# Performance work log

Measured on AMD Instinct MI355X. Metric: run time of the kernel, lower is better.

Reference implementation:

```python
import jax, jax.numpy as jnp
import numpy as np

B, N, D, H, C = 8, 1024, 1024, 8, 1
S = 32            # sqrt(D // C): per-patch spatial map side
HD = D // H       # head dim = 128
SCALE = HD ** -0.5
BN_EPS = 1e-3     # Keras BatchNormalization default epsilon


def setup_inputs() -> dict:
    key = jax.random.key(0)
    ks = jax.random.split(key, 7)
    std = 0.02  # matches tf.random_normal_initializer(0.0, 0.02)
    return {
        "x": jax.random.normal(ks[0], (B, N, D), jnp.float32),
        "qw": jax.random.normal(ks[1], (3, 3, C, C), jnp.float32) * std,
        "kw": jax.random.normal(ks[2], (3, 3, C, C), jnp.float32) * std,
        "vw": jax.random.normal(ks[3], (3, 3, C, C), jnp.float32) * std,
        "reatten_w": jax.random.normal(ks[4], (N, N), jnp.float32) / np.float32(np.sqrt(N)),
        "reatten_b": jnp.zeros((N,), jnp.float32),
        "bn_gamma": jnp.ones((N,), jnp.float32),
        "bn_beta": jnp.zeros((N,), jnp.float32),
        "proj_w": jax.random.normal(ks[5], (D, D), jnp.float32) / np.float32(np.sqrt(D)),
        "proj_b": jnp.zeros((D,), jnp.float32),
    }


def _conv_qkv(x, w):
    # unflatten: [B, N, D] -> [B*N, S, S, C]; map_fn over batch with a shared
    # conv == one conv with B*N as batch dim. 3x3 SAME, no bias, exact GELU.
    xm = x.reshape(B * N, S, S, C)
    y = jax.lax.conv_general_dilated(
        xm, w, window_strides=(1, 1), padding='SAME',
        dimension_numbers=('NHWC', 'HWIO', 'NHWC'))
    y = jax.nn.gelu(y, approximate=False)
    # reshape to heads: [B, N, H, HD] -> [B, H, N, HD]
    return y.reshape(B, N, H, HD).transpose(0, 2, 1, 3)


def reference(x, qw, kw, vw, reatten_w, reatten_b, bn_gamma, bn_beta, proj_w, proj_b):
    q = _conv_qkv(x, qw)
    k = _conv_qkv(x, kw)
    v = _conv_qkv(x, vw)

    attn = jax.nn.softmax(jnp.einsum('bhid,bhjd->bhij', q, k) * SCALE, axis=-1)
    # re-attention: 1x1 conv over last (key) axis + BN (inference: mean=0, var=1)
    attn = jnp.einsum('bhic,cj->bhij', attn, reatten_w) + reatten_b
    attn = attn * (bn_gamma / jnp.sqrt(jnp.float32(1.0) + BN_EPS)) + bn_beta
    # reatten_scale = 1.0 (transform_scale=False)

    out = jnp.einsum('bhij,bhjd->bhid', attn, v)
    out = out.transpose(0, 2, 1, 3).reshape(B, N, D)
    out = out @ proj_w + proj_b
    return (out, attn)
```

## Files before the change

kernel.cpp:

```cpp
#include <hip/hip_runtime.h>
#include <hip/hip_bf16.h>

typedef __attribute__((ext_vector_type(8))) short short8;
typedef __attribute__((ext_vector_type(4))) float f32x4;

__device__ __forceinline__ void gload_lds16(const void* g, void* l) {
    __builtin_amdgcn_global_load_lds(
        (const __attribute__((address_space(1))) void*)g,
        (__attribute__((address_space(3))) void*)l, 16, 0, 0);
}

__device__ __forceinline__ float gelu_exact(float x) {
    return 0.5f * x * (1.0f + erff(x * 0.70710678118654752f));
}
__device__ __forceinline__ unsigned short f2b_raw(float f) {
    __hip_bfloat16 h = __float2bfloat16(f);
    return *reinterpret_cast<unsigned short*>(&h);
}
__device__ __forceinline__ float tofloat(float f) { return f; }
__device__ __forceinline__ float tofloat(__hip_bfloat16 h) { return __bfloat162float(h); }

__global__ __launch_bounds__(256) void conv_qkv(
    const float* __restrict__ x,
    const float* __restrict__ qw, const float* __restrict__ kw, const float* __restrict__ vw,
    __hip_bfloat16* __restrict__ qb, __hip_bfloat16* __restrict__ kb, __hip_bfloat16* __restrict__ vb)
{
    __shared__ float img[1024];
    const int bid = blockIdx.x;
    const int b = bid >> 10, n = bid & 1023;
    const float* xr = x + (long)bid * 1024;
    for (int i = threadIdx.x; i < 1024; i += 256) img[i] = xr[i];
    __syncthreads();

    float wq[9], wk[9], wv[9];
    #pragma unroll
    for (int i = 0; i < 9; ++i) { wq[i] = qw[i]; wk[i] = kw[i]; wv[i] = vw[i]; }

    for (int q = 0; q < 4; ++q) {
        const int p = q * 256 + threadIdx.x;
        const int r = p >> 5, c = p & 31;
        float sq = 0.f, sk = 0.f, sv = 0.f;
        #pragma unroll
        for (int dy = 0; dy < 3; ++dy) {
            const int rr = r + dy - 1;
            if (rr < 0 || rr > 31) continue;
            #pragma unroll
            for (int dx = 0; dx < 3; ++dx) {
                const int cc = c + dx - 1;
                if (cc < 0 || cc > 31) continue;
                const float px = img[rr * 32 + cc];
                sq += px * wq[dy * 3 + dx];
                sk += px * wk[dy * 3 + dx];
                sv += px * wv[dy * 3 + dx];
            }
        }
        sq = gelu_exact(sq); sk = gelu_exact(sk); sv = gelu_exact(sv);
        const int h = p >> 7, d = p & 127;
        const long off = ((long)(b * 8 + h) * 1024 + n) * 128 + d;
        qb[off] = __float2bfloat16(sq);
        kb[off] = __float2bfloat16(sk);
        vb[off] = __float2bfloat16(sv);
    }
}

template <typename Tin>
__global__ __launch_bounds__(256) void transpose_cast(
    const Tin* __restrict__ in, __hip_bfloat16* __restrict__ out,
    int R, int Cc, long inz, long outz)
{
    __shared__ float tile[32][33];
    const long z = blockIdx.z;
    const int c0 = blockIdx.x * 32, r0 = blockIdx.y * 32;
    const int tx = threadIdx.x & 31, ty = threadIdx.x >> 5;
    const Tin* ip = in + z * inz;
    #pragma unroll
    for (int i = 0; i < 32; i += 8)
        tile[ty + i][tx] = tofloat(ip[(long)(r0 + ty + i) * Cc + (c0 + tx)]);
    __syncthreads();
    __hip_bfloat16* op = out + z * outz;
    #pragma unroll
    for (int i = 0; i < 32; i += 8)
        op[(long)(c0 + ty + i) * R + (r0 + tx)] = __float2bfloat16(tile[tx][ty + i]);
}

__global__ __launch_bounds__(256, 2) void qk_softmax(
    const __hip_bfloat16* __restrict__ qb, const __hip_bfloat16* __restrict__ kb,
    __hip_bfloat16* __restrict__ Pun, float* __restrict__ linv)
{
    __shared__ __align__(16) char smem[74240];
    char* As = smem;
    char* Bs = smem + 32768;
    __hip_bfloat16* pbuf = (__hip_bfloat16*)(smem + 65536);
    float* lred = (float*)(smem + 65536);

    const int tid = threadIdx.x;
    const int rt = blockIdx.x, z = blockIdx.y;
    const char* Ag = (const char*)(qb + ((long)z * 1024 + rt * 128) * 128);
    const char* Bg = (const char*)(kb + (long)z * 1024 * 128);

    int gsrc[8], pphys[8];
    #pragma unroll
    for (int i = 0; i < 8; ++i) {
        const int p = i * 4096 + tid * 16;
        const int L = p ^ (((p >> 8) & 7) << 4);
        pphys[i] = p; gsrc[i] = L;
    }
    auto STAGE = [&](const char* gb, char* lb) {
        #pragma unroll
        for (int i = 0; i < 8; ++i) gload_lds16(gb + gsrc[i], lb + pphys[i]);
    };
    auto LD8 = [&](const char* buf, int L) -> short8 {
        const int ph = L ^ (((L >> 8) & 7) << 4);
        return *(const short8*)(buf + ph);
    };

    const int lane = tid & 63, wave = tid >> 6;
    const int wr = (wave >> 1) * 64, wc = (wave & 1) * 64;
    const int fr = lane & 15, kl = lane >> 4;

    STAGE(Ag, As);
    STAGE(Bg, Bs);
    __syncthreads();

    short8 af[4][4];
    #pragma unroll
    for (int m = 0; m < 4; ++m)
        #pragma unroll
        for (int kk = 0; kk < 4; ++kk)
            af[m][kk] = LD8(As, (wr + m * 16 + fr) * 256 + (kl * 8 + kk * 32) * 2);

    float lacc[4][4];
    #pragma unroll
    for (int m = 0; m < 4; ++m)
        #pragma unroll
        for (int r = 0; r < 4; ++r) lacc[m][r] = 0.f;

    const float SCALE = 0.08838834764831843f;

    for (int c = 0; c < 8; ++c) {
        f32x4 acc[4][4];
        #pragma unroll
        for (int m = 0; m < 4; ++m)
            #pragma unroll
            for (int n = 0; n < 4; ++n) acc[m][n] = (f32x4){0.f, 0.f, 0.f, 0.f};

        #pragma unroll
        for (int kk = 0; kk < 4; ++kk) {
            short8 bf[4];
            #pragma unroll
            for (int n = 0; n < 4; ++n)
                bf[n] = LD8(Bs, (wc + n * 16 + fr) * 256 + (kl * 8 + kk * 32) * 2);
            #pragma unroll
            for (int m = 0; m < 4; ++m)
                #pragma unroll
                for (int n = 0; n < 4; ++n)
                    acc[m][n] = __builtin_amdgcn_mfma_f32_16x16x32_bf16(af[m][kk], bf[n], acc[m][n], 0, 0, 0);
        }

        #pragma unroll
        for (int m = 0; m < 4; ++m) {
            #pragma unroll
            for (int n = 0; n < 4; ++n)
                #pragma unroll
                for (int r = 0; r < 4; ++r)
                    acc[m][n][r] = __expf(acc[m][n][r] * SCALE);
            #pragma unroll
            for (int r = 0; r < 4; ++r)
                lacc[m][r] += (acc[m][0][r] + acc[m][1][r]) + (acc[m][2][r] + acc[m][3][r]);
        }

        #pragma unroll
        for (int q2 = 0; q2 < 4; ++q2) {
            if ((wave >> 1) == (q2 >> 1)) {
                #pragma unroll
                for (int mm = 0; mm < 2; ++mm) {
                    const int m = (q2 & 1) * 2 + mm;
                    const int lr0 = m * 16 + kl * 4 - (q2 & 1) * 32;
                    #pragma unroll
                    for (int n = 0; n < 4; ++n)
                        #pragma unroll
                        for (int r = 0; r < 4; ++r)
                            pbuf[(lr0 + r) * 136 + wc + n * 16 + fr] = __float2bfloat16(acc[m][n][r]);
                }
            }
            __syncthreads();
            #pragma unroll
            for (int p = 0; p < 2; ++p) {
                const int idx = (tid + p * 256) * 8;
                const int row = idx >> 7, col = idx & 127;
                short8 s = *(const short8*)&pbuf[row * 136 + col];
                *(short8*)&Pun[((long)z * 1024 + rt * 128 + q2 * 32 + row) * 1024 + c * 128 + col] = s;
            }
            __syncthreads();
        }

        if (c < 7) {
            STAGE(Bg + (c + 1) * 32768, Bs);
            __syncthreads();
        }
    }

    #pragma unroll
    for (int m = 0; m < 4; ++m)
        #pragma unroll
        for (int r = 0; r < 4; ++r) {
            float v = lacc[m][r];
            v += __shfl_xor(v, 1); v += __shfl_xor(v, 2);
            v += __shfl_xor(v, 4); v += __shfl_xor(v, 8);
            lacc[m][r] = v;
        }
    __syncthreads();
    if (fr == 0) {
        #pragma unroll
        for (int m = 0; m < 4; ++m)
            #pragma unroll
            for (int r = 0; r < 4; ++r)
                lred[(wr + m * 16 + kl * 4 + r) * 2 + (wave & 1)] = lacc[m][r];
    }
    __syncthreads();
    if (tid < 128) {
        const float s = lred[tid * 2] + lred[tid * 2 + 1];
        linv[(long)z * 1024 + rt * 128 + tid] = 1.0f / s;
    }
}

__global__ __launch_bounds__(512, 2) void gemm_reatten_256(
    const __hip_bfloat16* __restrict__ Sall, const __hip_bfloat16* __restrict__ Wt,
    float* __restrict__ Cout, __hip_bfloat16* __restrict__ C2out,
    const float* __restrict__ bg, const float* __restrict__ rb, const float* __restrict__ bb,
    const float* __restrict__ linv)
{
    __shared__ __align__(16) char smem[131072];
    char* ldsA = smem;
    char* ldsB = smem + 65536;

    const int tid = threadIdx.x;
    const int h = blockIdx.x + (blockIdx.y << 2) + (blockIdx.z << 4);
    const int lg = (h & 7) * 128 + (h >> 3);
    const int z = lg >> 4, tileM = lg & 3, tileN = (lg >> 2) & 3;

    const char* Ab = (const char*)(Sall + (long)z * 1048576 + (long)tileM * 256 * 1024);
    const char* Bb = (const char*)(Wt + (long)tileN * 256 * 1024);

    int grow[2], goff[2], pphys[2];
    #pragma unroll
    for (int i = 0; i < 2; ++i) {
        const int p = i * 8192 + tid * 16;
        const int l = p ^ (((p >> 7) & 3) << 4);
        pphys[i] = p; grow[i] = l >> 6; goff[i] = l & 63;
    }
    auto STAGE = [&](const char* gb, char* lb, int kt) {
        #pragma unroll
        for (int i = 0; i < 2; ++i)
            gload_lds16(gb + (long)grow[i] * 2048 + kt * 64 + goff[i], lb + pphys[i]);
    };

    const int lane = tid & 63, wid = tid >> 6;
    const int wrM = wid >> 2, wcn = wid & 3;
    const int fr = lane & 15, kl = lane >> 4;
    const int frbase = fr * 64 + kl * 16;

    auto LD8 = [&](const char* buf, int L) -> short8 {
        const int ph = L ^ (((L >> 7) & 3) << 4);
        return *(const short8*)(buf + ph);
    };

    f32x4 acc[8][4];
    #pragma unroll
    for (int m = 0; m < 8; ++m)
        #pragma unroll
        for (int n = 0; n < 4; ++n) acc[m][n] = (f32x4){0.f, 0.f, 0.f, 0.f};

    STAGE(Ab, ldsA, 0);          STAGE(Bb, ldsB, 0);
    STAGE(Ab, ldsA + 16384, 1);  STAGE(Bb, ldsB + 16384, 1);
    asm volatile("s_waitcnt vmcnt(4)" ::: "memory");
    __builtin_amdgcn_sched_barrier(0);
    __builtin_amdgcn_s_barrier();
    __builtin_amdgcn_sched_barrier(0);

    #pragma unroll 1
    for (int t = 0; t < 32; ++t) {
        char* bufA = ldsA + (t & 3) * 16384;
        char* bufB = ldsB + (t & 3) * 16384;
        const int t2 = t + 2;
        char* nA = ldsA + (t2 & 3) * 16384;
        char* nB = ldsB + (t2 & 3) * 16384;

        short8 bf[4], af[4], ag[4];
        #pragma unroll
        for (int n = 0; n < 4; ++n) bf[n] = LD8(bufB, ((wcn * 64 + n * 16) * 64) + frbase);
        #pragma unroll
        for (int j = 0; j < 4; ++j) af[j] = LD8(bufA, ((wrM * 128 + j * 16) * 64) + frbase);
        if (t2 < 32) STAGE(Ab, nA, t2);
        __builtin_amdgcn_s_setprio(1);
        #pragma unroll
        for (int j = 0; j < 4; ++j)
            #pragma unroll
            for (int n = 0; n < 4; ++n)
                acc[j][n] = __builtin_amdgcn_mfma_f32_16x16x32_bf16(af[j], bf[n], acc[j][n], 0, 0, 0);
        __builtin_amdgcn_s_setprio(0);

        #pragma unroll
        for (int j = 0; j < 4; ++j) ag[j] = LD8(bufA, ((wrM * 128 + 64 + j * 16) * 64) + frbase);
        if (t2 < 32) STAGE(Bb, nB, t2);
        __builtin_amdgcn_s_setprio(1);
        #pragma unroll
        for (int j = 0; j < 4; ++j)
            #pragma unroll
            for (int n = 0; n < 4; ++n)
                acc[4 + j][n] = __builtin_amdgcn_mfma_f32_16x16x32_bf16(ag[j], bf[n], acc[4 + j][n], 0, 0, 0);
        __builtin_amdgcn_s_setprio(0);

        if (t < 30)       { asm volatile("s_waitcnt vmcnt(4)" ::: "memory"); }
        else if (t == 30) { asm volatile("s_waitcnt vmcnt(0)" ::: "memory"); }
        __builtin_amdgcn_sched_barrier(0);
        __builtin_amdgcn_s_barrier();
        __builtin_amdgcn_sched_barrier(0);
    }

    __syncthreads();
    float* cbuf = (float*)smem;
    const float bninv = rsqrtf(1.0f + 1e-3f);
    float alpha[4], addv[4];
    #pragma unroll
    for (int n = 0; n < 4; ++n) {
        const int col = tileN * 256 + wcn * 64 + n * 16 + fr;
        const float g = bg[col];
        alpha[n] = g * bninv;
        addv[n] = rb[col] * alpha[n] + bb[col];
    }
    const float* linvz = linv + (long)z * 1024 + tileM * 256 + wrM * 128 + kl * 4;
    f32x4 lr[8];
    #pragma unroll
    for (int mf = 0; mf < 8; ++mf) lr[mf] = *(const f32x4*)(linvz + mf * 16);

    const int srow = tid >> 3, cseg = (tid & 7) * 4, c8 = (tid & 7) * 8;
    #pragma unroll
    for (int c = 0; c < 4; ++c) {
        if (wrM == (c >> 1)) {
            #pragma unroll
            for (int j = 0; j < 4; ++j) {
                const int mf = (c & 1) * 4 + j;
                const int lrow0 = j * 16 + kl * 4;
                #pragma unroll
                for (int n = 0; n < 4; ++n)
                    #pragma unroll
                    for (int r = 0; r < 4; ++r)
                        cbuf[(lrow0 + r) * 260 + wcn * 64 + n * 16 + fr] =
                            acc[mf][n][r] * (lr[mf][r] * alpha[n]) + addv[n];
            }
        }
        __syncthreads();
        const long gro = (long)(tileM * 256 + c * 64 + srow);
        float* gp = Cout + (long)z * 1048576 + gro * 1024 + tileN * 256;
        #pragma unroll
        for (int i = 0; i < 8; ++i)
            *(f32x4*)(gp + cseg + i * 32) = *(const f32x4*)&cbuf[srow * 260 + cseg + i * 32];
        __hip_bfloat16* gp2 = C2out + (long)z * 1048576 + gro * 1024 + tileN * 256;
        #pragma unroll
        for (int i = 0; i < 4; ++i) {
            const float* src = &cbuf[srow * 260 + c8 + i * 64];
            f32x4 v0 = *(const f32x4*)src;
            f32x4 v1 = *(const f32x4*)(src + 4);
            short8 s;
            #pragma unroll
            for (int k = 0; k < 4; ++k) {
                s[k] = (short)f2b_raw(v0[k]);
                s[k + 4] = (short)f2b_raw(v1[k]);
            }
            *(short8*)(gp2 + c8 + i * 64) = s;
        }
        __syncthreads();
    }
}

template <int MODE>
__global__ __launch_bounds__(256) void gemm_nt(
    const __hip_bfloat16* __restrict__ Aall, const __hip_bfloat16* __restrict__ Ball,
    void* __restrict__ Call, int K,
    long sAz, long sBz, long sCz,
    const float* __restrict__ e0)
{
    constexpr bool OF32 = (MODE == 3);

    __shared__ __align__(16) char smem[32 * 132 * 4];
    short* As = (short*)smem;
    short* Bs = (short*)(smem + 8192);
    float* cbuf = (float*)smem;

    const int tid = threadIdx.x;
    const int z = blockIdx.z;
    const int tileM = blockIdx.x, tileN = blockIdx.y;

    const short* Aw = (const short*)Aall + sAz * z + (long)tileM * 128 * K;
    const short* Bw = (const short*)Ball + sBz * z + (long)tileN * 128 * K;

    const int r0s = tid >> 2, k0s = (tid & 3) * 8;
    const int r1s = r0s + 64;

    f32x4 acc[4][4];
    #pragma unroll
    for (int m = 0; m < 4; ++m)
        #pragma unroll
        for (int n = 0; n < 4; ++n) acc[m][n] = (f32x4){0.f, 0.f, 0.f, 0.f};

    const int lane = tid & 63;
    const int wave = tid >> 6;
    const int wr = (wave >> 1) * 64, wc = (wave & 1) * 64;
    const int fr = lane & 15;
    const int kb = (lane >> 4) * 8;

    const int nk = K >> 5;
    for (int kt = 0; kt < nk; ++kt) {
        __syncthreads();
        gload_lds16(Aw + (long)r0s * K + kt * 32 + k0s, &As[tid * 8]);
        gload_lds16(Aw + (long)r1s * K + kt * 32 + k0s, &As[(tid + 256) * 8]);
        gload_lds16(Bw + (long)r0s * K + kt * 32 + k0s, &Bs[tid * 8]);
        gload_lds16(Bw + (long)r1s * K + kt * 32 + k0s, &Bs[(tid + 256) * 8]);
        __syncthreads();

        short8 af[4], bf[4];
        #pragma unroll
        for (int m = 0; m < 4; ++m) af[m] = *(const short8*)&As[(wr + m * 16 + fr) * 32 + kb];
        #pragma unroll
        for (int n = 0; n < 4; ++n) bf[n] = *(const short8*)&Bs[(wc + n * 16 + fr) * 32 + kb];
        #pragma unroll
        for (int m = 0; m < 4; ++m)
            #pragma unroll
            for (int n = 0; n < 4; ++n)
                acc[m][n] = __builtin_amdgcn_mfma_f32_16x16x32_bf16(af[m], bf[n], acc[m][n], 0, 0, 0);
    }

    long cbase;
    if (MODE == 2) cbase = (long)(z >> 3) * 1048576 + (long)(z & 7) * 128;
    else           cbase = sCz * z;

    float addv[4];
    #pragma unroll
    for (int n = 0; n < 4; ++n) {
        const int col = tileN * 128 + wc + n * 16 + fr;
        addv[n] = (MODE == 3) ? e0[col] : 0.f;
    }

    __syncthreads();
    #pragma unroll
    for (int q = 0; q < 4; ++q) {
        if ((wave >> 1) == (q >> 1)) {
            #pragma unroll
            for (int mm = 0; mm < 2; ++mm) {
                const int m = (q & 1) * 2 + mm;
                const int lr0 = m * 16 + (lane >> 4) * 4 - (q & 1) * 32;
                #pragma unroll
                for (int n = 0; n < 4; ++n)
                    #pragma unroll
                    for (int r = 0; r < 4; ++r)
                        cbuf[(lr0 + r) * 132 + wc + n * 16 + fr] = acc[m][n][r] + addv[n];
            }
        }
        __syncthreads();
        const long growbase = (long)tileM * 128 + q * 32;
        if constexpr (OF32) {
            float* Cg = (float*)Call + cbase;
            #pragma unroll
            for (int pass = 0; pass < 4; ++pass) {
                const int idx = (tid + pass * 256) * 4;
                const int row = idx >> 7, col = idx & 127;
                f32x4 v = *(const f32x4*)&cbuf[row * 132 + col];
                *(f32x4*)&Cg[(growbase + row) * 1024 + tileN * 128 + col] = v;
            }
        } else {
            __hip_bfloat16* Cg = (__hip_bfloat16*)Call + cbase;
            #pragma unroll
            for (int pass = 0; pass < 2; ++pass) {
                const int idx = (tid + pass * 256) * 8;
                const int row = idx >> 7, col = idx & 127;
                const float* src = &cbuf[row * 132 + col];
                f32x4 v0 = *(const f32x4*)src;
                f32x4 v1 = *(const f32x4*)(src + 4);
                short8 s;
                #pragma unroll
                for (int i = 0; i < 4; ++i) {
                    s[i] = (short)f2b_raw(v0[i]);
                    s[i + 4] = (short)f2b_raw(v1[i]);
                }
                *(short8*)&Cg[(growbase + row) * 1024 + tileN * 128 + col] = s;
            }
        }
        __syncthreads();
    }
}

extern "C" void kernel_launch(void* const* d_in, const int* in_sizes, int n_in,
                              void* d_out, int out_size, void* d_ws, size_t ws_size,
                              hipStream_t stream)
{
    const float* x  = (const float*)d_in[0];
    const float* qw = (const float*)d_in[1];
    const float* kw = (const float*)d_in[2];
    const float* vw = (const float*)d_in[3];
    const float* rw = (const float*)d_in[4];
    const float* rb = (const float*)d_in[5];
    const float* bg = (const float*)d_in[6];
    const float* bb = (const float*)d_in[7];
    const float* pw = (const float*)d_in[8];
    const float* pb = (const float*)d_in[9];

    float* outF  = (float*)d_out;
    float* attnF = outF + 8388608;

    char* w = (char*)d_ws;
    __hip_bfloat16* qb    = (__hip_bfloat16*)w; w += 16777216;
    __hip_bfloat16* kb    = (__hip_bfloat16*)w; w += 16777216;
    __hip_bfloat16* vb    = (__hip_bfloat16*)w; w += 16777216;
    __hip_bfloat16* vt    = (__hip_bfloat16*)w; w += 16777216;
    __hip_bfloat16* Wt    = (__hip_bfloat16*)w; w += 2097152;
    __hip_bfloat16* pWt   = (__hip_bfloat16*)w; w += 2097152;
    __hip_bfloat16* o2    = (__hip_bfloat16*)w; w += 16777216;
    float*          linv  = (float*)w;          w += 262144;
    __hip_bfloat16* Pun   = (__hip_bfloat16*)w; w += 134217728;
    __hip_bfloat16* attnb = (__hip_bfloat16*)w; w += 134217728;

    conv_qkv<<<8192, 256, 0, stream>>>(x, qw, kw, vw, qb, kb, vb);
    transpose_cast<float><<<dim3(32, 32, 1), 256, 0, stream>>>(rw, Wt, 1024, 1024, 0, 0);
    transpose_cast<float><<<dim3(32, 32, 1), 256, 0, stream>>>(pw, pWt, 1024, 1024, 0, 0);
    transpose_cast<__hip_bfloat16><<<dim3(4, 32, 64), 256, 0, stream>>>(vb, vt, 1024, 128, 131072, 131072);

    qk_softmax<<<dim3(8, 64), 256, 0, stream>>>(qb, kb, Pun, linv);
    gemm_reatten_256<<<dim3(4, 4, 64), 512, 0, stream>>>(Pun, Wt, attnF, attnb, bg, rb, bb, linv);
    gemm_nt<2><<<dim3(8, 1, 64), 256, 0, stream>>>(
        attnb, vt, o2, 1024, 1048576, 131072, 0, nullptr);
    gemm_nt<3><<<dim3(64, 8, 1), 256, 0, stream>>>(
        o2, pWt, outF, 1024, 0, 0, 0, pb);
}
```

Before: 397.4 us.

## Restructure reatten GEMM to double-buffered K=64 stages with plain block mapping

The reatten GEMM kernel moves from a 4-deep ring of K=32 LDS stages, with two loads in flight and explicit vmcnt waits, to a double-buffered scheme of K=64 stages. It runs 16 iterations with a wider XOR swizzle and __syncthreads between iterations. The swizzled grid-to-tile remapping is replaced by a direct blockIdx mapping, and launch bounds drop the two-blocks-per-CU hint. This cuts barrier count and loop overhead, but it gives up one stage of prefetch depth and the L2-locality remap, and the full-barrier waits may expose more load latency.

```diff
diff --git a/kernel.cpp b/kernel.cpp
--- a/kernel.cpp
+++ b/kernel.cpp
@@ -224,7 +224,7 @@
     }
 }
 
-__global__ __launch_bounds__(512, 2) void gemm_reatten_256(
+__global__ __launch_bounds__(512, 1) void gemm_reatten_256(
     const __hip_bfloat16* __restrict__ Sall, const __hip_bfloat16* __restrict__ Wt,
     float* __restrict__ Cout, __hip_bfloat16* __restrict__ C2out,
     const float* __restrict__ bg, const float* __restrict__ rb, const float* __restrict__ bb,
@@ -235,33 +235,29 @@
     char* ldsB = smem + 65536;
 
     const int tid = threadIdx.x;
-    const int h = blockIdx.x + (blockIdx.y << 2) + (blockIdx.z << 4);
-    const int lg = (h & 7) * 128 + (h >> 3);
-    const int z = lg >> 4, tileM = lg & 3, tileN = (lg >> 2) & 3;
-
+    const int z = blockIdx.z, tileM = blockIdx.x, tileN = blockIdx.y;
     const char* Ab = (const char*)(Sall + (long)z * 1048576 + (long)tileM * 256 * 1024);
     const char* Bb = (const char*)(Wt + (long)tileN * 256 * 1024);
 
-    int grow[2], goff[2], pphys[2];
-    #pragma unroll
-    for (int i = 0; i < 2; ++i) {
+    int gsrow[4], gscol[4], pphys[4];
+    #pragma unroll
+    for (int i = 0; i < 4; ++i) {
         const int p = i * 8192 + tid * 16;
-        const int l = p ^ (((p >> 7) & 3) << 4);
-        pphys[i] = p; grow[i] = l >> 6; goff[i] = l & 63;
+        const int L = p ^ (((p >> 7) & 7) << 4);
+        pphys[i] = p; gsrow[i] = L >> 7; gscol[i] = L & 127;
     }
     auto STAGE = [&](const char* gb, char* lb, int kt) {
         #pragma unroll
-        for (int i = 0; i < 2; ++i)
-            gload_lds16(gb + (long)grow[i] * 2048 + kt * 64 + goff[i], lb + pphys[i]);
+        for (int i = 0; i < 4; ++i)
+            gload_lds16(gb + (long)gsrow[i] * 2048 + kt * 128 + gscol[i], lb + pphys[i]);
     };
 
     const int lane = tid & 63, wid = tid >> 6;
     const int wrM = wid >> 2, wcn = wid & 3;
     const int fr = lane & 15, kl = lane >> 4;
-    const int frbase = fr * 64 + kl * 16;
 
     auto LD8 = [&](const char* buf, int L) -> short8 {
-        const int ph = L ^ (((L >> 7) & 3) << 4);
+        const int ph = L ^ (((L >> 7) & 7) << 4);
         return *(const short8*)(buf + ph);
     };
 
@@ -271,54 +267,58 @@
         #pragma unroll
         for (int n = 0; n < 4; ++n) acc[m][n] = (f32x4){0.f, 0.f, 0.f, 0.f};
 
-    STAGE(Ab, ldsA, 0);          STAGE(Bb, ldsB, 0);
-    STAGE(Ab, ldsA + 16384, 1);  STAGE(Bb, ldsB + 16384, 1);
-    asm volatile("s_waitcnt vmcnt(4)" ::: "memory");
-    __builtin_amdgcn_sched_barrier(0);
-    __builtin_amdgcn_s_barrier();
-    __builtin_amdgcn_sched_barrier(0);
+    STAGE(Ab, ldsA, 0);
+    STAGE(Bb, ldsB, 0);
+    __syncthreads();
 
     #pragma unroll 1
-    for (int t = 0; t < 32; ++t) {
-        char* bufA = ldsA + (t & 3) * 16384;
-        char* bufB = ldsB + (t & 3) * 16384;
-        const int t2 = t + 2;
-        char* nA = ldsA + (t2 & 3) * 16384;
-        char* nB = ldsB + (t2 & 3) * 16384;
-
-        short8 bf[4], af[4], ag[4];
-        #pragma unroll
-        for (int n = 0; n < 4; ++n) bf[n] = LD8(bufB, ((wcn * 64 + n * 16) * 64) + frbase);
-        #pragma unroll
-        for (int j = 0; j < 4; ++j) af[j] = LD8(bufA, ((wrM * 128 + j * 16) * 64) + frbase);
-        if (t2 < 32) STAGE(Ab, nA, t2);
+    for (int t = 0; t < 16; ++t) {
+        char* bufA = ldsA + (t & 1) * 32768;
+        char* bufB = ldsB + (t & 1) * 32768;
+        char* nA = ldsA + ((t + 1) & 1) * 32768;
+        char* nB = ldsB + ((t + 1) & 1) * 32768;
+
+        short8 bf[4][2], af[4][2];
+        #pragma unroll
+        for (int n = 0; n < 4; ++n)
+            #pragma unroll
+            for (int ks = 0; ks < 2; ++ks)
+                bf[n][ks] = LD8(bufB, (wcn * 64 + n * 16 + fr) * 128 + ks * 64 + kl * 16);
+        #pragma unroll
+        for (int j = 0; j < 4; ++j)
+            #pragma unroll
+            for (int ks = 0; ks < 2; ++ks)
+                af[j][ks] = LD8(bufA, (wrM * 128 + j * 16 + fr) * 128 + ks * 64 + kl * 16);
+        if (t < 15) STAGE(Ab, nA, t + 1);
         __builtin_amdgcn_s_setprio(1);
         #pragma unroll
         for (int j = 0; j < 4; ++j)
             #pragma unroll
-            for (int n = 0; n < 4; ++n)
-                acc[j][n] = __builtin_amdgcn_mfma_f32_16x16x32_bf16(af[j], bf[n], acc[j][n], 0, 0, 0);
+            for (int n = 0; n < 4; ++n) {
+                acc[j][n] = __builtin_amdgcn_mfma_f32_16x16x32_bf16(af[j][0], bf[n][0], acc[j][n], 0, 0, 0);
+                acc[j][n] = __builtin_amdgcn_mfma_f32_16x16x32_bf16(af[j][1], bf[n][1], acc[j][n], 0, 0, 0);
+            }
         __builtin_amdgcn_s_setprio(0);
 
         #pragma unroll
-        for (int j = 0; j < 4; ++j) ag[j] = LD8(bufA, ((wrM * 128 + 64 + j * 16) * 64) + frbase);
-        if (t2 < 32) STAGE(Bb, nB, t2);
+        for (int j = 0; j < 4; ++j)
+            #pragma unroll
+            for (int ks = 0; ks < 2; ++ks)
+                af[j][ks] = LD8(bufA, (wrM * 128 + 64 + j * 16 + fr) * 128 + ks * 64 + kl * 16);
+        if (t < 15) STAGE(Bb, nB, t + 1);
         __builtin_amdgcn_s_setprio(1);
         #pragma unroll
         for (int j = 0; j < 4; ++j)
             #pragma unroll
-            for (int n = 0; n < 4; ++n)
-                acc[4 + j][n] = __builtin_amdgcn_mfma_f32_16x16x32_bf16(ag[j], bf[n], acc[4 + j][n], 0, 0, 0);
+            for (int n = 0; n < 4; ++n) {
+                acc[4 + j][n] = __builtin_amdgcn_mfma_f32_16x16x32_bf16(af[j][0], bf[n][0], acc[4 + j][n], 0, 0, 0);
+                acc[4 + j][n] = __builtin_amdgcn_mfma_f32_16x16x32_bf16(af[j][1], bf[n][1], acc[4 + j][n], 0, 0, 0);
+            }
         __builtin_amdgcn_s_setprio(0);
 
-        if (t < 30)       { asm volatile("s_waitcnt vmcnt(4)" ::: "memory"); }
-        else if (t == 30) { asm volatile("s_waitcnt vmcnt(0)" ::: "memory"); }
-        __builtin_amdgcn_sched_barrier(0);
-        __builtin_amdgcn_s_barrier();
-        __builtin_amdgcn_sched_barrier(0);
-    }
-
-    __syncthreads();
+        __syncthreads();
+    }
+
     float* cbuf = (float*)smem;
     const float bninv = rsqrtf(1.0f + 1e-3f);
     float alpha[4], addv[4];
```

After: 376.2 us. -5.3%, faster.
